# Performance work log

Hardware: AMD Instinct MI355X
Metric: run time of the kernel (lower is better)

The kernel has to match this reference:

```python
import jax, jax.numpy as jnp
import numpy as np

B, D, H, W, C = 1, 16, 56, 56, 256
WD, WH, WW = 2, 7, 7
SD, SH, SW = 1, 3, 3
HEADS = 8
HDIM = C // HEADS
N = WD * WH * WW          # 98 tokens per window
NW = (D // WD) * (H // WH) * (W // WW)  # 512 windows per batch element
HID = 4 * C


def _rel_index():
    coords = np.stack(np.meshgrid(np.arange(WD), np.arange(WH), np.arange(WW), indexing='ij')).reshape(3, -1)
    rel = (coords[:, :, None] - coords[:, None, :]).transpose(1, 2, 0).astype(np.int64)
    rel[..., 0] += WD - 1; rel[..., 1] += WH - 1; rel[..., 2] += WW - 1
    rel[..., 0] *= (2 * WH - 1) * (2 * WW - 1)
    rel[..., 1] *= (2 * WW - 1)
    return rel.sum(-1)  # (N, N)

REL_INDEX = jnp.asarray(_rel_index())


def _np_window_partition(x):
    b, d, h, w, c = x.shape
    x = x.reshape(b, d // WD, WD, h // WH, WH, w // WW, WW, c)
    return x.transpose(0, 1, 3, 5, 2, 4, 6, 7).reshape(-1, N, c)


def _compute_mask():
    # Swin compute_mask: label 3x3x3 shifted regions, windows mask cross-region pairs with -100
    img = np.zeros((1, D, H, W, 1), np.float32)
    cnt = 0
    for ds in (slice(0, -WD), slice(-WD, -SD), slice(-SD, None)):
        for hs in (slice(0, -WH), slice(-WH, -SH), slice(-SH, None)):
            for ws in (slice(0, -WW), slice(-WW, -SW), slice(-SW, None)):
                img[:, ds, hs, ws, :] = cnt; cnt += 1
    mw = _np_window_partition(img).reshape(NW, N)
    am = mw[:, None, :] - mw[:, :, None]
    return np.where(am != 0, -100.0, 0.0).astype(np.float32)


def setup_inputs():
    key = jax.random.key(0)
    ks = jax.random.split(key, 8)
    s = 0.02
    return {
        'x': jax.random.normal(ks[0], (B, D, H, W, C), jnp.float32),
        'mask_matrix': jnp.asarray(_compute_mask()),
        'g1': jnp.ones((C,), jnp.float32), 'b1': jnp.zeros((C,), jnp.float32),
        'qkv_w': jax.random.normal(ks[1], (C, 3 * C), jnp.float32) * s,
        'qkv_b': jnp.zeros((3 * C,), jnp.float32),
        'rpb': jax.random.normal(ks[2], ((2 * WD - 1) * (2 * WH - 1) * (2 * WW - 1), HEADS), jnp.float32) * s,
        'proj_w': jax.random.normal(ks[3], (C, C), jnp.float32) * s,
        'proj_b': jnp.zeros((C,), jnp.float32),
        'g2': jnp.ones((C,), jnp.float32), 'b2': jnp.zeros((C,), jnp.float32),
        'fc1_w': jax.random.normal(ks[4], (C, HID), jnp.float32) * s,
        'fc1_b': jnp.zeros((HID,), jnp.float32),
        'fc2_w': jax.random.normal(ks[5], (HID, C), jnp.float32) * s,
        'fc2_b': jnp.zeros((C,), jnp.float32),
    }


def _ln(x, g, b):
    mu = jnp.mean(x, -1, keepdims=True)
    var = jnp.mean((x - mu) ** 2, -1, keepdims=True)
    return (x - mu) * jax.lax.rsqrt(var + 1e-5) * g + b


def _window_partition(x):
    b = x.shape[0]
    x = x.reshape(b, D // WD, WD, H // WH, WH, W // WW, WW, C)
    return x.transpose(0, 1, 3, 5, 2, 4, 6, 7).reshape(-1, N, C)


def _window_reverse(w):
    x = w.reshape(B, D // WD, H // WH, W // WW, WD, WH, WW, C)
    return x.transpose(0, 1, 4, 2, 5, 3, 6, 7).reshape(B, D, H, W, C)


def reference(x, mask_matrix, g1, b1, qkv_w, qkv_b, rpb, proj_w, proj_b, g2, b2, fc1_w, fc1_b, fc2_w, fc2_b):
    shortcut = x
    y = _ln(x, g1, b1)
    # D,H,W divide window sizes -> pad amounts are 0; cyclic shift for SW-MSA
    y = jnp.roll(y, shift=(-SD, -SH, -SW), axis=(1, 2, 3))
    xw = _window_partition(y)                          # (B_, N, C)
    B_ = xw.shape[0]
    qkv = (xw @ qkv_w + qkv_b).reshape(B_, N, 3, HEADS, HDIM)
    q, k, v = jnp.moveaxis(qkv, 2, 0)                  # each (B_, N, HEADS, HDIM)
    q = q * (HDIM ** -0.5)
    attn = jnp.einsum('bnhd,bmhd->bhnm', q, k)         # (B_, HEADS, N, N)
    bias = rpb[REL_INDEX.reshape(-1)].reshape(N, N, HEADS).transpose(2, 0, 1)
    attn = attn + bias[None]
    attn = attn.reshape(B_ // NW, NW, HEADS, N, N) + mask_matrix[None, :, None]
    attn = jax.nn.softmax(attn.reshape(B_, HEADS, N, N), axis=-1)
    out = jnp.einsum('bhnm,bmhd->bnhd', attn, v).reshape(B_, N, C)
    out = out @ proj_w + proj_b
    y = _window_reverse(out)
    y = jnp.roll(y, shift=(SD, SH, SW), axis=(1, 2, 3))
    x = shortcut + y
    h = _ln(x, g2, b2)
    h = jax.nn.gelu(h @ fc1_w + fc1_b, approximate=False)
    h = h @ fc2_w + fc2_b
    return x + h
```

## Files before the change

### kernel.cpp

```cpp
#include <hip/hip_runtime.h>
#include <hip/hip_bf16.h>

typedef __hip_bfloat16 bf16;
typedef __attribute__((ext_vector_type(4))) float f32x4;
typedef __attribute__((ext_vector_type(8))) short bf16x8;

#define MFMA16(a,b,c) __builtin_amdgcn_mfma_f32_16x16x32_bf16((a),(b),(c),0,0,0)

static __device__ inline unsigned short bfbits(float f) {
  __hip_bfloat16 h = __float2bfloat16(f);
  union { __hip_bfloat16 h; unsigned short u; } u;
  u.h = h; return u.u;
}
static __device__ inline float bf2f(unsigned short u) {
  return __uint_as_float(((unsigned int)u) << 16);
}
static __device__ inline void gld16(const void* g, void* l) {
  __builtin_amdgcn_global_load_lds((const __attribute__((address_space(1))) void*)g,
                                   (__attribute__((address_space(3))) void*)l, 16, 0, 0);
}

__global__ __launch_bounds__(256) void prep_k(const float* __restrict__ qkv_w,
                                              const float* __restrict__ proj_w,
                                              const float* __restrict__ fc1_w,
                                              const float* __restrict__ fc2_w,
                                              const float* __restrict__ rpb,
                                              bf16* __restrict__ wqkvT,
                                              bf16* __restrict__ wprojT,
                                              bf16* __restrict__ wfc1T,
                                              bf16* __restrict__ wfc2T,
                                              unsigned short* __restrict__ biasT,
                                              unsigned int* __restrict__ rowoff0,
                                              unsigned int* __restrict__ rowmap1) {
  const int b = blockIdx.x, tid = threadIdx.x;
  if (b < 768) {
    int idx = b * 256 + tid;
    int n = idx >> 8, k = idx & 255;
    float v = qkv_w[k * 768 + n];
    if (n < 256) v *= 0.17677669529663687f;
    wqkvT[idx] = __float2bfloat16(v);
  } else if (b < 1024) {
    int idx = (b - 768) * 256 + tid;
    int n = idx >> 8, k = idx & 255;
    wprojT[idx] = __float2bfloat16(proj_w[k * 256 + n]);
  } else if (b < 2048) {
    int idx = (b - 1024) * 256 + tid;
    int n = idx >> 8, k = idx & 255;
    wfc1T[idx] = __float2bfloat16(fc1_w[k * 1024 + n]);
  } else if (b < 3072) {
    int idx = (b - 2048) * 256 + tid;
    int n = idx >> 10, k = idx & 1023;
    wfc2T[idx] = __float2bfloat16(fc2_w[k * 256 + n]);
  } else if (b < 3110) {
    int idx = (b - 3072) * 256 + tid;
    if (idx < 9604) {
      int nn = idx / 98, mm = idx - nn * 98;
      int ld = nn / 49, lrem = nn - ld * 49, lh = lrem / 7, lw = lrem - lh * 7;
      int md = mm / 49, mrem = mm - md * 49, mh = mrem / 7, mw = mrem - mh * 7;
      int rel = (ld - md + 1) * 169 + (lh - mh + 6) * 13 + (lw - mw + 6);
      #pragma unroll
      for (int h = 0; h < 8; ++h)
        biasT[h * 9604 + mm * 98 + nn] = bfbits(rpb[rel * 8 + h]);
    }
  } else {
    int row = (b - 3110) * 256 + tid;
    if (row < 50176) {
      int widx = row / 98, n = row - widx * 98;
      rowoff0[row] = (unsigned int)(widx * 25088 + n * 32);
      int zd = widx >> 6, zh = (widx >> 3) & 7, zw = widx & 7;
      int ld = n / 49, rem = n - ld * 49, lh = rem / 7, lw = rem - lh * 7;
      int d = zd * 2 + ld, h = zh * 7 + lh, w = zw * 7 + lw;
      int dsrc = (d + 1) & 15;
      int hsrc = h + 3; if (hsrc >= 56) hsrc -= 56;
      int wsrc = w + 3; if (wsrc >= 56) wsrc -= 56;
      rowmap1[row] = (unsigned int)((dsrc * 56 + hsrc) * 56 + wsrc);
    }
  }
}

__global__ __launch_bounds__(256) void vtrans_k(const unsigned short* __restrict__ v,
                                                unsigned short* __restrict__ vt) {
  __shared__ unsigned short S[98 * 33];
  const unsigned short* src = v + (size_t)blockIdx.x * 3136;
  for (int i = threadIdx.x; i < 3136; i += 256) {
    int n = i >> 5, d = i & 31;
    S[n * 33 + d] = src[i];
  }
  __syncthreads();
  unsigned short* dst = vt + ((size_t)blockIdx.x << 12);
  for (int i = threadIdx.x; i < 4096; i += 256) {
    int d = i >> 7, m = i & 127;
    dst[i] = (m < 98) ? S[m * 33 + d] : (unsigned short)0;
  }
}

__global__ __launch_bounds__(256) void ln_k(const float* __restrict__ x,
                                            const float* __restrict__ g,
                                            const float* __restrict__ bias,
                                            bf16* __restrict__ out, int windowed) {
  const int wid = threadIdx.x >> 6, lane = threadIdx.x & 63;
  const int t = blockIdx.x * 4 + wid;
  int src = t;
  if (windowed) {
    int widx = t / 98, n = t - widx * 98;
    int zd = widx >> 6, zh = (widx >> 3) & 7, zw = widx & 7;
    int ld = n / 49, rem = n - ld * 49, lh = rem / 7, lw = rem - lh * 7;
    int d = zd * 2 + ld, h = zh * 7 + lh, w = zw * 7 + lw;
    int dsrc = (d + 1) & 15;
    int hsrc = h + 3; if (hsrc >= 56) hsrc -= 56;
    int wsrc = w + 3; if (wsrc >= 56) wsrc -= 56;
    src = (dsrc * 56 + hsrc) * 56 + wsrc;
  }
  const float4 v = *(const float4*)(x + (size_t)src * 256 + lane * 4);
  float s1 = v.x + v.y + v.z + v.w;
  float s2 = v.x * v.x + v.y * v.y + v.z * v.z + v.w * v.w;
  #pragma unroll
  for (int d = 1; d < 64; d <<= 1) {
    s1 += __shfl_xor(s1, d);
    s2 += __shfl_xor(s2, d);
  }
  float mu = s1 * (1.f / 256.f);
  float var = s2 * (1.f / 256.f) - mu * mu;
  float rs = rsqrtf(var + 1e-5f);
  const float4 gv = *(const float4*)(g + lane * 4);
  const float4 bv = *(const float4*)(bias + lane * 4);
  ushort4 pk;
  pk.x = bfbits((v.x - mu) * rs * gv.x + bv.x);
  pk.y = bfbits((v.y - mu) * rs * gv.y + bv.y);
  pk.z = bfbits((v.z - mu) * rs * gv.z + bv.z);
  pk.w = bfbits((v.w - mu) * rs * gv.w + bv.w);
  *(ushort4*)((unsigned short*)out + (size_t)t * 256 + lane * 4) = pk;
}

template<int EPI>
__global__ __launch_bounds__(256) void gemm_k(const bf16* __restrict__ A,
                                              const bf16* __restrict__ Bt,
                                              const float* __restrict__ bias,
                                              int N, int K, int NX, int mrow0,
                                              bf16* __restrict__ out_bf,
                                              float* __restrict__ out_f,
                                              const float* __restrict__ add_f,
                                              const unsigned int* __restrict__ rmap) {
  __shared__ bf16 As[2][128 * 32];
  __shared__ bf16 Bs[2][128 * 32];
  const int tid = threadIdx.x;
  const int wid = tid >> 6, lane = tid & 63;
  const int q8 = gridDim.x >> 3;
  const int tile = (blockIdx.x & 7) * q8 + (blockIdx.x >> 3);
  const int bx = tile % NX, by = tile / NX;
  const int row0 = by * 128, col0 = bx * 128;
  const int lrow = tid >> 2, lcol = (tid & 3) * 8;
  const int fr = lane & 15, kh = lane >> 4;
  const int wm = (wid >> 1) * 64, wn = (wid & 1) * 64;
  f32x4 zero4 = {0.f, 0.f, 0.f, 0.f};
  f32x4 acc[4][4];
  #pragma unroll
  for (int i = 0; i < 4; ++i)
    #pragma unroll
    for (int j = 0; j < 4; ++j) acc[i][j] = zero4;

  const bf16* aP = A + (size_t)(row0 + lrow) * K + lcol;
  const bf16* bP = Bt + (size_t)(col0 + lrow) * K + lcol;
  bf16* asD = &As[0][lrow * 32 + lcol];
  bf16* bsD = &Bs[0][lrow * 32 + lcol];

  const int nk = K >> 5;
  gld16(aP, asD);
  gld16(aP + (size_t)64 * K, asD + 2048);
  gld16(bP, bsD);
  gld16(bP + (size_t)64 * K, bsD + 2048);

  int cur = 0;
  for (int t = 0; t < nk; ++t) {
    __syncthreads();
    if (t + 1 < nk) {
      int k0 = (t + 1) * 32;
      bf16* aD = asD + (cur ^ 1) * 4096;
      bf16* bD = bsD + (cur ^ 1) * 4096;
      gld16(aP + k0, aD);
      gld16(aP + (size_t)64 * K + k0, aD + 2048);
      gld16(bP + k0, bD);
      gld16(bP + (size_t)64 * K + k0, bD + 2048);
    }
    const bf16* Ab = As[cur];
    const bf16* Bb = Bs[cur];
    bf16x8 af[4], bfr[4];
    #pragma unroll
    for (int i = 0; i < 4; ++i)
      af[i] = *(const bf16x8*)&Ab[(wm + i * 16 + fr) * 32 + kh * 8];
    #pragma unroll
    for (int j = 0; j < 4; ++j)
      bfr[j] = *(const bf16x8*)&Bb[(wn + j * 16 + fr) * 32 + kh * 8];
    #pragma unroll
    for (int i = 0; i < 4; ++i)
      #pragma unroll
      for (int j = 0; j < 4; ++j)
        acc[i][j] = MFMA16(af[i], bfr[j], acc[i][j]);
    cur ^= 1;
  }

  #pragma unroll
  for (int i = 0; i < 4; ++i) {
    #pragma unroll
    for (int r = 0; r < 4; ++r) {
      int row = row0 + wm + i * 16 + kh * 4 + r;
      unsigned int rl = (EPI == 0 || EPI == 1) ? rmap[row] : 0u;
      #pragma unroll
      for (int j = 0; j < 4; ++j) {
        int col = col0 + wn + j * 16 + fr;
        float bb = bias[col];
        if (EPI == 0 && col < 256) bb *= 0.17677669529663687f;
        float v = acc[i][j][r] + bb;
        if (EPI == 0) {
          int part = col >> 8, head = (col >> 5) & 7, hd = col & 31;
          size_t off = (size_t)part * 12845056 + rl + head * 3136 + hd;
          out_bf[off] = __float2bfloat16(v);
        } else if (EPI == 1) {
          size_t tok = rl;
          out_f[tok * 256 + col] = add_f[tok * 256 + col] + v;
        } else if (EPI == 2) {
          float gl = 0.5f * v * (1.0f + erff(v * 0.70710678118654752f));
          out_bf[(size_t)row * 1024 + col] = __float2bfloat16(gl);
        } else {
          size_t ro = (size_t)(mrow0 + row);
          out_f[ro * 256 + col] = add_f[ro * 256 + col] + v;
        }
      }
    }
  }
}

__global__ __launch_bounds__(256, 2) void attn_k(const bf16* __restrict__ qkv,
                                                 const unsigned short* __restrict__ vt,
                                                 const unsigned short* __restrict__ bias_bf,
                                                 bf16* __restrict__ out) {
  __shared__ unsigned short Pl[112 * 128];
  __shared__ unsigned short biasS[112 * 100];
  __shared__ float invS[112];
  __shared__ unsigned char lblS[112];
  const int tid = threadIdx.x;
  const int widx = blockIdx.x >> 1, hh = blockIdx.x & 1;
  const int wid = tid >> 6, lane = tid & 63;
  const int fr = lane & 15, kh = lane >> 4, kh4 = kh * 4;
  const int tr0 = wid * 2;
  f32x4 zero4 = {0.f, 0.f, 0.f, 0.f};

  if (tid < 112) {
    unsigned char l = 255;
    if (tid < 98) {
      int zd = widx >> 6, zh = (widx >> 3) & 7, zw = widx & 7;
      int ld = tid / 49, rem = tid - ld * 49, lh = rem / 7, lw = rem - lh * 7;
      int d = zd * 2 + ld, h = zh * 7 + lh, w = zw * 7 + lw;
      int cd = (d >= 14) + (d >= 15);
      int ch = (h >= 49) + (h >= 53);
      int cw = (w >= 49) + (w >= 53);
      l = (unsigned char)(cd * 9 + ch * 3 + cw);
    }
    lblS[tid] = l;
  }
  __syncthreads();

  unsigned int lblK[7];
  #pragma unroll
  for (int mt = 0; mt < 7; ++mt)
    lblK[mt] = *(const unsigned int*)&lblS[mt * 16 + kh4];
  const bool t1v = (tr0 + 1) < 7;
  unsigned int lq0 = 0x01010101u * lblS[tr0 * 16 + fr];
  unsigned int lq1 = 0x01010101u * lblS[(t1v ? tr0 + 1 : 0) * 16 + fr];

  for (int it = 0; it < 4; ++it) {
    const int head = hh * 4 + it;
    const unsigned short* qbu = (const unsigned short*)qkv + ((size_t)widx * 8 + head) * 3136;
    const unsigned short* kbu = qbu + (size_t)12845056;
    const unsigned short* brow = bias_bf + head * 9604;
    const unsigned short* vtb = vt + (((size_t)widx * 8 + head) << 12);

    __syncthreads();
    for (int j = tid; j < 4802; j += 256) {
      int n = j / 49, m2 = (j - n * 49) * 2;
      *(unsigned int*)&biasS[n * 100 + m2] = *(const unsigned int*)(brow + n * 98 + m2);
    }
    for (int j = tid; j < 700; j += 256) {
      int n = j / 50, m2 = (j - n * 50) * 2;
      *(unsigned int*)&biasS[(98 + n) * 100 + m2] = 0xFF80FF80u;
    }

    int qr0 = tr0 * 16 + fr; if (qr0 > 97) qr0 = 97;
    int qr1 = (tr0 + 1) * 16 + fr; if (qr1 > 97) qr1 = 97;
    bf16x8 aq0 = *(const bf16x8*)(qbu + qr0 * 32 + kh * 8);
    bf16x8 aq1 = *(const bf16x8*)(qbu + qr1 * 32 + kh * 8);

    f32x4 s2[2][7];
    #pragma unroll
    for (int a = 0; a < 2; ++a)
      #pragma unroll
      for (int m = 0; m < 7; ++m) s2[a][m] = zero4;
    #pragma unroll
    for (int mt = 0; mt < 7; ++mt) {
      int krow = mt * 16 + fr; if (krow > 97) krow = 97;
      bf16x8 kf = *(const bf16x8*)(kbu + krow * 32 + kh * 8);
      s2[0][mt] = MFMA16(kf, aq0, s2[0][mt]);
      s2[1][mt] = MFMA16(kf, aq1, s2[1][mt]);
    }
    __syncthreads();

    #pragma unroll
    for (int ti = 0; ti < 2; ++ti) {
      int tr = tr0 + ti;
      if (tr < 7) {
        int q = tr * 16 + fr;
        int qc = (q < 98) ? q : 0;
        unsigned int lq = (ti == 0) ? lq0 : lq1;
        float mxa = -1e30f, mxb = -1e30f;
        #pragma unroll
        for (int mt = 0; mt < 7; ++mt) {
          unsigned int df = lblK[mt] ^ lq;
          #pragma unroll
          for (int r = 0; r < 4; ++r) {
            int k = mt * 16 + kh4 + r;
            float b = bf2f(biasS[k * 100 + qc]);
            float msk = ((df >> (8 * r)) & 255u) ? -100.f : 0.f;
            s2[ti][mt][r] = s2[ti][mt][r] + b + msk;
          }
          mxa = fmaxf(mxa, fmaxf(s2[ti][mt][0], s2[ti][mt][1]));
          mxb = fmaxf(mxb, fmaxf(s2[ti][mt][2], s2[ti][mt][3]));
        }
        float mx = fmaxf(mxa, mxb);
        mx = fmaxf(mx, __shfl_xor(mx, 16));
        mx = fmaxf(mx, __shfl_xor(mx, 32));
        float suma = 0.f, sumb = 0.f;
        #pragma unroll
        for (int mt = 0; mt < 7; ++mt) {
          float e0 = __expf(s2[ti][mt][0] - mx);
          float e1 = __expf(s2[ti][mt][1] - mx);
          float e2 = __expf(s2[ti][mt][2] - mx);
          float e3 = __expf(s2[ti][mt][3] - mx);
          s2[ti][mt][0] = e0; s2[ti][mt][1] = e1;
          s2[ti][mt][2] = e2; s2[ti][mt][3] = e3;
          suma += e0 + e1; sumb += e2 + e3;
        }
        float sum = suma + sumb;
        sum += __shfl_xor(sum, 16);
        sum += __shfl_xor(sum, 32);
        if (kh == 0) invS[q] = 1.0f / sum;
        #pragma unroll
        for (int mt = 0; mt < 7; ++mt) {
          ushort4 pk;
          pk.x = bfbits(s2[ti][mt][0]);
          pk.y = bfbits(s2[ti][mt][1]);
          pk.z = bfbits(s2[ti][mt][2]);
          pk.w = bfbits(s2[ti][mt][3]);
          *(ushort4*)&Pl[(q * 128 + mt * 16 + kh4) ^ ((q & 7) << 3)] = pk;
        }
        ushort4 zz; zz.x = zz.y = zz.z = zz.w = 0;
        *(ushort4*)&Pl[(q * 128 + 112 + kh4) ^ ((q & 7) << 3)] = zz;
      }
    }

    f32x4 o00 = zero4, o01 = zero4, o10 = zero4, o11 = zero4;
    #pragma unroll
    for (int kk = 0; kk < 4; ++kk) {
      bf16x8 vv0 = *(const bf16x8*)(vtb + fr * 128 + kk * 32 + kh * 8);
      bf16x8 vv1 = *(const bf16x8*)(vtb + (16 + fr) * 128 + kk * 32 + kh * 8);
      int prow0 = tr0 * 16 + fr;
      bf16x8 pa0 = *(const bf16x8*)&((const bf16*)Pl)[(prow0 * 128 + kk * 32 + kh * 8) ^ ((prow0 & 7) << 3)];
      o00 = MFMA16(pa0, vv0, o00);
      o01 = MFMA16(pa0, vv1, o01);
      if (t1v) {
        int prow1 = prow0 + 16;
        bf16x8 pa1 = *(const bf16x8*)&((const bf16*)Pl)[(prow1 * 128 + kk * 32 + kh * 8) ^ ((prow1 & 7) << 3)];
        o10 = MFMA16(pa1, vv0, o10);
        o11 = MFMA16(pa1, vv1, o11);
      }
    }
    #pragma unroll
    for (int r = 0; r < 4; ++r) {
      int row = tr0 * 16 + kh4 + r;
      if (row < 98) {
        float iv = invS[row];
        size_t grow = (size_t)widx * 98 + row;
        out[grow * 256 + head * 32 + fr] = __float2bfloat16(o00[r] * iv);
        out[grow * 256 + head * 32 + 16 + fr] = __float2bfloat16(o01[r] * iv);
      }
    }
    if (t1v) {
      #pragma unroll
      for (int r = 0; r < 4; ++r) {
        int row = (tr0 + 1) * 16 + kh4 + r;
        if (row < 98) {
          float iv = invS[row];
          size_t grow = (size_t)widx * 98 + row;
          out[grow * 256 + head * 32 + fr] = __float2bfloat16(o10[r] * iv);
          out[grow * 256 + head * 32 + 16 + fr] = __float2bfloat16(o11[r] * iv);
        }
      }
    }
  }
}

extern "C" void kernel_launch(void* const* d_in, const int* in_sizes, int n_in,
                              void* d_out, int out_size, void* d_ws, size_t ws_size,
                              hipStream_t stream) {
  const float* x      = (const float*)d_in[0];
  const float* g1     = (const float*)d_in[2];
  const float* b1     = (const float*)d_in[3];
  const float* qkv_w  = (const float*)d_in[4];
  const float* qkv_b  = (const float*)d_in[5];
  const float* rpb    = (const float*)d_in[6];
  const float* proj_w = (const float*)d_in[7];
  const float* proj_b = (const float*)d_in[8];
  const float* g2     = (const float*)d_in[9];
  const float* b2     = (const float*)d_in[10];
  const float* fc1_w  = (const float*)d_in[11];
  const float* fc1_b  = (const float*)d_in[12];
  const float* fc2_w  = (const float*)d_in[13];
  const float* fc2_b  = (const float*)d_in[14];
  float* outp = (float*)d_out;

  char* ws = (char*)d_ws;
  if (ws_size < (size_t)156237824) return;
  bf16*  wqkvT   = (bf16*)(ws + 0);
  bf16*  wprojT  = (bf16*)(ws + 393216);
  bf16*  wfc1T   = (bf16*)(ws + 524288);
  bf16*  wfc2T   = (bf16*)(ws + 1048576);
  unsigned short* bias_bf = (unsigned short*)(ws + 1572864);
  unsigned int* rowmap1 = (unsigned int*)(ws + 1726528);
  float* x2      = (float*)(ws + 2097152);
  unsigned int* rowoff0 = (unsigned int*)(ws + 2097152);
  unsigned short* vtb = (unsigned short*)(ws + 11931648);
  char*  pool    = ws + 53477376;
  bf16*  xw       = (bf16*)pool;
  bf16*  qkvb     = (bf16*)(pool + 25690112);
  bf16*  attn_out = (bf16*)pool;
  bf16*  hbuf     = (bf16*)pool;
  bf16*  hh       = (bf16*)(pool + 25690112);

  prep_k<<<3307, 256, 0, stream>>>(qkv_w, proj_w, fc1_w, fc2_w, rpb,
                                   wqkvT, wprojT, wfc1T, wfc2T, bias_bf,
                                   rowoff0, rowmap1);

  ln_k<<<12544, 256, 0, stream>>>(x, g1, b1, xw, 1);
  gemm_k<0><<<2352, 256, 0, stream>>>(xw, wqkvT, qkv_b, 768, 256, 6, 0,
                                      qkvb, nullptr, nullptr, rowoff0);
  vtrans_k<<<4096, 256, 0, stream>>>((const unsigned short*)qkvb + (size_t)2 * 12845056, vtb);
  attn_k<<<1024, 256, 0, stream>>>(qkvb, vtb, bias_bf, attn_out);
  gemm_k<1><<<784, 256, 0, stream>>>(attn_out, wprojT, proj_b, 256, 256, 2, 0,
                                     nullptr, x2, x, rowmap1);
  ln_k<<<12544, 256, 0, stream>>>(x2, g2, b2, hbuf, 0);
  for (int ch = 0; ch < 2; ++ch) {
    gemm_k<2><<<1568, 256, 0, stream>>>(hbuf + (size_t)ch * 25088 * 256, wfc1T, fc1_b,
                                        1024, 256, 8, 0, hh, nullptr, nullptr, nullptr);
    gemm_k<3><<<392, 256, 0, stream>>>(hh, wfc2T, fc2_b, 256, 1024, 2, ch * 25088,
                                       nullptr, outp, x2, nullptr);
  }
}
```

Baseline: 304.9 us.

## Widen GEMM tiles to 128x256 with 512-thread blocks and balanced XCD mapping

The GEMM kernel now runs 8 waves per block over a 128x256 output tile instead of 4 waves over 128x128. Each A tile in LDS is reused across twice as many columns, and all grid sizes and NX values are halved to match. The XCD tile remapping now handles grid sizes not divisible by 8. The cost is more LDS per block and fewer blocks, which can hurt occupancy and wave balance. The fc2 GEMM in particular now launches only 196 blocks.

```diff
diff --git a/kernel.cpp b/kernel.cpp
--- a/kernel.cpp
+++ b/kernel.cpp
@@ -133,7 +133,7 @@
 }
 
 template<int EPI>
-__global__ __launch_bounds__(256) void gemm_k(const bf16* __restrict__ A,
+__global__ __launch_bounds__(512) void gemm_k(const bf16* __restrict__ A,
                                               const bf16* __restrict__ Bt,
                                               const float* __restrict__ bias,
                                               int N, int K, int NX, int mrow0,
@@ -142,16 +142,16 @@
                                               const float* __restrict__ add_f,
                                               const unsigned int* __restrict__ rmap) {
   __shared__ bf16 As[2][128 * 32];
-  __shared__ bf16 Bs[2][128 * 32];
+  __shared__ bf16 Bs[2][256 * 32];
   const int tid = threadIdx.x;
   const int wid = tid >> 6, lane = tid & 63;
-  const int q8 = gridDim.x >> 3;
-  const int tile = (blockIdx.x & 7) * q8 + (blockIdx.x >> 3);
+  const int nwg = gridDim.x, xcd = blockIdx.x & 7, o8 = blockIdx.x >> 3;
+  const int qq = nwg >> 3, r8 = nwg & 7;
+  const int tile = (xcd < r8 ? xcd * (qq + 1) : r8 * (qq + 1) + (xcd - r8) * qq) + o8;
   const int bx = tile % NX, by = tile / NX;
-  const int row0 = by * 128, col0 = bx * 128;
-  const int lrow = tid >> 2, lcol = (tid & 3) * 8;
+  const int row0 = by * 128, col0 = bx * 256;
   const int fr = lane & 15, kh = lane >> 4;
-  const int wm = (wid >> 1) * 64, wn = (wid & 1) * 64;
+  const int wm = (wid >> 2) * 64, wn = (wid & 3) * 64;
   f32x4 zero4 = {0.f, 0.f, 0.f, 0.f};
   f32x4 acc[4][4];
   #pragma unroll
@@ -159,28 +159,28 @@
     #pragma unroll
     for (int j = 0; j < 4; ++j) acc[i][j] = zero4;
 
-  const bf16* aP = A + (size_t)(row0 + lrow) * K + lcol;
-  const bf16* bP = Bt + (size_t)(col0 + lrow) * K + lcol;
-  bf16* asD = &As[0][lrow * 32 + lcol];
-  bf16* bsD = &Bs[0][lrow * 32 + lcol];
+  const int srow = tid >> 2, sq = (tid & 3) * 8;
+  const bf16* aP = A + (size_t)(row0 + srow) * K + sq;
+  const bf16* bP = Bt + (size_t)(col0 + srow) * K + sq;
+  const bf16* bP2 = Bt + (size_t)(col0 + srow + 128) * K + sq;
+  bf16* asD = &As[0][srow * 32 + sq];
+  bf16* bsD = &Bs[0][srow * 32 + sq];
+  bf16* bsD2 = &Bs[0][(srow + 128) * 32 + sq];
 
   const int nk = K >> 5;
   gld16(aP, asD);
-  gld16(aP + (size_t)64 * K, asD + 2048);
   gld16(bP, bsD);
-  gld16(bP + (size_t)64 * K, bsD + 2048);
+  gld16(bP2, bsD2);
 
   int cur = 0;
   for (int t = 0; t < nk; ++t) {
     __syncthreads();
     if (t + 1 < nk) {
       int k0 = (t + 1) * 32;
-      bf16* aD = asD + (cur ^ 1) * 4096;
-      bf16* bD = bsD + (cur ^ 1) * 4096;
-      gld16(aP + k0, aD);
-      gld16(aP + (size_t)64 * K + k0, aD + 2048);
-      gld16(bP + k0, bD);
-      gld16(bP + (size_t)64 * K + k0, bD + 2048);
+      int so = (cur ^ 1);
+      gld16(aP + k0, asD + so * 4096);
+      gld16(bP + k0, bsD + so * 8192);
+      gld16(bP2 + k0, bsD2 + so * 8192);
     }
     const bf16* Ab = As[cur];
     const bf16* Bb = Bs[cur];
@@ -440,17 +440,17 @@
                                    rowoff0, rowmap1);
 
   ln_k<<<12544, 256, 0, stream>>>(x, g1, b1, xw, 1);
-  gemm_k<0><<<2352, 256, 0, stream>>>(xw, wqkvT, qkv_b, 768, 256, 6, 0,
+  gemm_k<0><<<1176, 512, 0, stream>>>(xw, wqkvT, qkv_b, 768, 256, 3, 0,
                                       qkvb, nullptr, nullptr, rowoff0);
   vtrans_k<<<4096, 256, 0, stream>>>((const unsigned short*)qkvb + (size_t)2 * 12845056, vtb);
   attn_k<<<1024, 256, 0, stream>>>(qkvb, vtb, bias_bf, attn_out);
-  gemm_k<1><<<784, 256, 0, stream>>>(attn_out, wprojT, proj_b, 256, 256, 2, 0,
+  gemm_k<1><<<392, 512, 0, stream>>>(attn_out, wprojT, proj_b, 256, 256, 1, 0,
                                      nullptr, x2, x, rowmap1);
   ln_k<<<12544, 256, 0, stream>>>(x2, g2, b2, hbuf, 0);
   for (int ch = 0; ch < 2; ++ch) {
-    gemm_k<2><<<1568, 256, 0, stream>>>(hbuf + (size_t)ch * 25088 * 256, wfc1T, fc1_b,
-                                        1024, 256, 8, 0, hh, nullptr, nullptr, nullptr);
-    gemm_k<3><<<392, 256, 0, stream>>>(hh, wfc2T, fc2_b, 256, 1024, 2, ch * 25088,
+    gemm_k<2><<<784, 512, 0, stream>>>(hbuf + (size_t)ch * 25088 * 256, wfc1T, fc1_b,
+                                       1024, 256, 4, 0, hh, nullptr, nullptr, nullptr);
+    gemm_k<3><<<196, 512, 0, stream>>>(hh, wfc2T, fc2_b, 256, 1024, 1, ch * 25088,
                                        nullptr, outp, x2, nullptr);
   }
 }
```

After: 307.1 us. Within noise of the previous version (+0.7%).
